# Optimization experiments

Hardware: AMD Instinct MI355X
Metric: run time of the kernel (lower is better)

The kernel has to match this reference:

```python
import jax, jax.numpy as jnp
import numpy as np

QDEPTH = 8
WIDTH = 64
HEIGHT = 64
WIRES = 12  # ceil(log2(64*64))
BATCH = 1024


def setup_inputs() -> dict:
    key = jax.random.key(0)
    k1, k2 = jax.random.split(key)
    x = jax.random.normal(k1, (BATCH, 1, WIDTH, HEIGHT), dtype=jnp.float32)
    # torch.nn.Parameter(torch.randn(weight_shape) * 0.4)
    weights = jax.random.normal(k2, (QDEPTH, WIRES, 3), dtype=jnp.float32) * 0.4
    return {"x": x, "weights": weights, "reps": 1}


def _rot_matrices(angles):
    # angles: (L, W, 3) -> (L, W, 2, 2) complex64; Rot(phi, theta, omega) = RZ(omega) RY(theta) RZ(phi)
    phi, theta, omega = angles[..., 0], angles[..., 1], angles[..., 2]
    c = jnp.cos(theta * 0.5).astype(jnp.complex64)
    s = jnp.sin(theta * 0.5).astype(jnp.complex64)
    ep = jnp.exp(-0.5j * (phi + omega).astype(jnp.complex64))  # e^{-i(phi+omega)/2}
    em = jnp.exp(-0.5j * (phi - omega).astype(jnp.complex64))  # e^{-i(phi-omega)/2}
    row0 = jnp.stack([ep * c, -jnp.conj(em) * s], axis=-1)
    row1 = jnp.stack([em * s, jnp.conj(ep) * c], axis=-1)
    return jnp.stack([row0, row1], axis=-2)


def _apply_1q(state, U, wire):
    # state: (B, 2, 2, ..., 2); apply 2x2 U on axis wire+1
    ax = wire + 1
    s = jnp.moveaxis(state, ax, -1)
    s = s @ U.T  # out[..., i] = sum_j U[i, j] s[..., j]
    return jnp.moveaxis(s, -1, ax)


def _apply_cnot(state, control, target):
    c, t = control + 1, target + 1
    s0, s1 = jnp.split(state, 2, axis=c)   # control = 0 / 1 halves
    s1 = jnp.flip(s1, axis=t)              # X on target where control = 1
    return jnp.concatenate([s0, s1], axis=c)


def _sel_layer(state, mats_l, r):
    # one StronglyEntanglingLayers layer: Rot on every wire, then CNOT ring of range r
    for w in range(WIRES):
        state = _apply_1q(state, mats_l[w], w)
    for w in range(WIRES):
        state = _apply_cnot(state, w, (w + r) % WIRES)
    return state


def _circuit(state, weights, reps):
    mats = _rot_matrices(jnp.tanh(weights))  # qw_map.tanh applied to raw weights
    for _ in range(reps):
        for l in range(QDEPTH):
            r = (l % (WIRES - 1)) + 1  # PennyLane default ranges
            layer = jax.checkpoint(lambda s, m, _r=r: _sel_layer(s, m, _r))
            state = layer(state, mats[l])
    return state


def reference(x, weights, reps):
    b = x.shape[0]
    v = x.reshape(b, -1)  # (b, 4096)
    norm = jnp.linalg.norm(v, axis=-1, keepdims=True)
    v = (v / norm).astype(jnp.complex64)
    state = v.reshape((b,) + (2,) * WIRES)
    state = _circuit(state, weights, reps)
    out = state.reshape(b, -1) * norm
    return out.reshape(b, 1, WIDTH, HEIGHT)
```

## Files before the change

### kernel.cpp

```cpp
#include <hip/hip_runtime.h>

#define WIRES   12
#define NSTATE  4096
#define QDEPTH  8
#define BLOCK   256
#define PER_T   16

using f2 = __attribute__((ext_vector_type(2))) float;

constexpr int colF(int l, int j) {
    int rr = (l % (WIRES - 1)) + 1;
    int v = 1 << j;
    for (int k = WIRES - 1; k >= 0; --k) {
        int bc = 11 - k;
        int bt = 11 - ((k + rr) % WIRES);
        v ^= ((v >> bc) & 1) << bt;
    }
    return v;
}

constexpr int sigma_c(int x) {
    int p = ((x >> 6) & 15) | (((x >> 10) & 3) << 4) | ((x & 63) << 6);
    return p ^ (((p >> 4) & 7) << 1);
}
struct SColsT { int v[QDEPTH][WIRES]; };
constexpr SColsT mkSCols() {
    SColsT c{};
    for (int l = 0; l < QDEPTH; ++l)
        for (int j = 0; j < WIRES; ++j) c.v[l][j] = sigma_c(colF(l, j));
    return c;
}
static __device__ const SColsT SCOLS = mkSCols();

#define OFF_KP 288
#define OFF_KW 544
#define OFF_AN 800

__global__ void setup_kernel(const float* __restrict__ wts, f2* __restrict__ mg)
{
    const int t = threadIdx.x;
    if (t < QDEPTH * WIRES) {
        float th = tanhf(wts[t * 3 + 1]);
        float c = cosf(0.5f * th), s = sinf(0.5f * th);
        mg[(t / 12) * 36 + (t % 12) * 3 + 0] = f2{ c,  c};
        mg[(t / 12) * 36 + (t % 12) * 3 + 1] = f2{-s, -s};
        mg[(t / 12) * 36 + (t % 12) * 3 + 2] = f2{ s,  s};
    }
    if (t < 64) {
        int l = t >> 3, j = t & 7;
        float aP = 0.5f * tanhf(wts[(l * 12 + (7 - j)) * 3 + 0]);
        int wj = (j == 0) ? 1 : (j == 1) ? 0 : (13 - j);
        float aW = 0.5f * tanhf(wts[(l * 12 + wj) * 3 + 2]);
        mg[OFF_AN + l * 8 + j] = f2{aP, aW};
    }
    {
        int l = t >> 5, k = (t >> 1) & 15;
        bool isW = (t & 1) != 0;
        float ph = 0.f;
        #pragma unroll
        for (int j = 0; j < 4; ++j) {
            int wire = isW ? (5 - j) : (11 - j);
            int comp = isW ? 2 : 0;
            float a  = 0.5f * tanhf(wts[(l * 12 + wire) * 3 + comp]);
            ph += ((k >> j) & 1) ? a : -a;
        }
        float s, c;
        sincosf(ph, &s, &c);
        int base = isW ? OFF_KW : OFF_KP;
        mg[base + l * 32 + k * 2 + 0] = f2{ c, c};
        mg[base + l * 32 + k * 2 + 1] = f2{-s, s};
    }
}

template<int P>
__device__ __forceinline__ void gateR(f2 r[PER_T], f2 cc, f2 ms, f2 ss)
{
    #pragma unroll
    for (int pr = 0; pr < PER_T / 2; pr += 2) {
        const int k0 = ((pr >> P) << (P + 1)) | (pr & ((1 << P) - 1));
        const int k1 = k0 | (1 << P);
        const int q  = pr + 1;
        const int j0 = ((q >> P) << (P + 1)) | (q & ((1 << P) - 1));
        const int j1 = j0 | (1 << P);
        f2 a0, b0, a1, b1;
        asm("v_pk_mul_f32 %0, %4, %8\n\t"
            "v_pk_mul_f32 %1, %4, %10\n\t"
            "v_pk_mul_f32 %2, %6, %8\n\t"
            "v_pk_mul_f32 %3, %6, %10\n\t"
            "v_pk_fma_f32 %0, %5, %9, %0\n\t"
            "v_pk_fma_f32 %1, %5, %8, %1\n\t"
            "v_pk_fma_f32 %2, %7, %9, %2\n\t"
            "v_pk_fma_f32 %3, %7, %8, %3"
            : "=&v"(a0), "=&v"(b0), "=&v"(a1), "=&v"(b1)
            : "v"(r[k0]), "v"(r[k1]), "v"(r[j0]), "v"(r[j1]),
              "v"(cc), "v"(ms), "v"(ss));
        r[k0] = a0; r[k1] = b0; r[j0] = a1; r[j1] = b1;
    }
}

template<int CTRL>
__device__ __forceinline__ f2 dpp_xor(f2 v) {
    f2 o;
    o.x = __int_as_float(__builtin_amdgcn_update_dpp(
            0, __float_as_int(v.x), CTRL, 0xF, 0xF, true));
    o.y = __int_as_float(__builtin_amdgcn_update_dpp(
            0, __float_as_int(v.y), CTRL, 0xF, 0xF, true));
    return o;
}

template<int CTRL>
__device__ __forceinline__ void dgateR(f2 r[PER_T], f2 cc, f2 k2)
{
    #pragma unroll
    for (int k0 = 0; k0 < PER_T; k0 += 4) {
        f2 p0 = dpp_xor<CTRL>(r[k0 + 0]);
        f2 p1 = dpp_xor<CTRL>(r[k0 + 1]);
        f2 p2 = dpp_xor<CTRL>(r[k0 + 2]);
        f2 p3 = dpp_xor<CTRL>(r[k0 + 3]);
        f2 o0, o1, o2, o3;
        asm("v_pk_mul_f32 %0, %4, %12\n\t"
            "v_pk_mul_f32 %1, %5, %12\n\t"
            "v_pk_mul_f32 %2, %6, %12\n\t"
            "v_pk_mul_f32 %3, %7, %12\n\t"
            "v_pk_fma_f32 %0, %8, %13, %0\n\t"
            "v_pk_fma_f32 %1, %9, %13, %1\n\t"
            "v_pk_fma_f32 %2, %10, %13, %2\n\t"
            "v_pk_fma_f32 %3, %11, %13, %3"
            : "=&v"(o0), "=&v"(o1), "=&v"(o2), "=&v"(o3)
            : "v"(r[k0]), "v"(r[k0+1]), "v"(r[k0+2]), "v"(r[k0+3]),
              "v"(p0), "v"(p1), "v"(p2), "v"(p3),
              "v"(cc), "v"(k2));
        r[k0] = o0; r[k0+1] = o1; r[k0+2] = o2; r[k0+3] = o3;
    }
}

__device__ __forceinline__ void dmul2(f2& a0, f2& a1, f2 d0r, f2 d0w,
                                      f2 d1r, f2 d1w)
{
    f2 o0, o1;
    asm("v_pk_mul_f32 %0, %2, %4\n\t"
        "v_pk_mul_f32 %1, %3, %6\n\t"
        "v_pk_fma_f32 %0, %2, %5, %0 op_sel:[1,0,0] op_sel_hi:[0,1,1]\n\t"
        "v_pk_fma_f32 %1, %3, %7, %1 op_sel:[1,0,0] op_sel_hi:[0,1,1]"
        : "=&v"(o0), "=&v"(o1)
        : "v"(a0), "v"(a1), "v"(d0r), "v"(d0w), "v"(d1r), "v"(d1w));
    a0 = o0; a1 = o1;
}

__device__ __forceinline__ void diag(f2 r[PER_T], const f2* __restrict__ AN,
                                     const f2* __restrict__ KF, int g, bool isW)
{
    float ph = 0.f;
    #pragma unroll
    for (int j = 0; j < 8; ++j) {
        float a = isW ? AN[j].y : AN[j].x;
        ph += ((g >> j) & 1) ? a : -a;
    }
    float s, c;
    sincosf(ph, &s, &c);
    const f2 Lr = f2{c, c}, Lw = f2{-s, s};
    #pragma unroll
    for (int k = 0; k < PER_T; k += 2)
        dmul2(r[k], r[k + 1], Lr, Lw, Lr, Lw);
    #pragma unroll
    for (int k = 0; k < PER_T; k += 2)
        dmul2(r[k], r[k + 1], KF[2*k], KF[2*k + 1], KF[2*k + 2], KF[2*k + 3]);
}

__global__ __launch_bounds__(BLOCK, 4) void qsim_kernel(
    const float* __restrict__ x,
    const f2*    __restrict__ mg,
    const int*   __restrict__ reps_ptr,
    float*       __restrict__ out,
    int write_mode)
{
    __shared__ alignas(16) f2 st[4096];
    float4* const stv = (float4*)st;

    const int g = threadIdx.x;
    const int b = blockIdx.x;
    const bool hb0 = (g & 1) != 0;
    const bool hb1 = (g & 2) != 0;

    const int Pg  = ((g >> 2) & 15) | (((g >> 6) & 3) << 4) | ((g & 3) << 10);
    const int B0W = Pg ^ (((g >> 6) & 3) << 1);
    const int B1W = B0W ^ 8;
    const int baseR4 = ((g & 3) << 3) | ((g >> 2) << 5);
    const int hj     = g & 7;

    const float4* xb4 = (const float4*)(x + (size_t)b * NSTATE) + g * 4;
    f2 r[PER_T];
    #pragma unroll
    for (int c = 0; c < 4; ++c) {
        float4 v = xb4[c];
        r[4*c+0] = f2{v.x, 0.f};
        r[4*c+1] = f2{v.y, 0.f};
        r[4*c+2] = f2{v.z, 0.f};
        r[4*c+3] = f2{v.w, 0.f};
    }

    const int reps = reps_ptr[0];
    for (int rep = 0; rep < reps; ++rep) {
        #pragma unroll 1
        for (int l = 0; l < QDEPTH; ++l) {
            const f2* CS = mg + l * 36;
            const f2* KP = mg + OFF_KP + l * 32;
            const f2* KW = mg + OFF_KW + l * 32;
            const f2* AN = mg + OFF_AN + l * 8;

            diag(r, AN, KP, g, false);

            gateR<0>(r, CS[11*3], CS[11*3+1], CS[11*3+2]);
            gateR<1>(r, CS[10*3], CS[10*3+1], CS[10*3+2]);
            gateR<2>(r, CS[9*3],  CS[9*3+1],  CS[9*3+2]);
            gateR<3>(r, CS[8*3],  CS[8*3+1],  CS[8*3+2]);
            dgateR<0xB1>(r, CS[7*3], hb0 ? CS[7*3+2] : CS[7*3+1]);
            dgateR<0x4E>(r, CS[6*3], hb1 ? CS[6*3+2] : CS[6*3+1]);

            #pragma unroll
            for (int k = 0; k < PER_T; ++k)
                st[((k & 1) ? B1W : B0W) + (k << 6)] = r[k];
            __syncthreads();

            #pragma unroll
            for (int j = 0; j < 8; ++j) {
                float4 v = stv[baseR4 | (j ^ hj)];
                r[2*j]     = f2{v.x, v.y};
                r[2*j + 1] = f2{v.z, v.w};
            }

            gateR<0>(r, CS[5*3], CS[5*3+1], CS[5*3+2]);
            gateR<1>(r, CS[4*3], CS[4*3+1], CS[4*3+2]);
            gateR<2>(r, CS[3*3], CS[3*3+1], CS[3*3+2]);
            gateR<3>(r, CS[2*3], CS[2*3+1], CS[2*3+2]);
            dgateR<0xB1>(r, CS[1*3], hb0 ? CS[1*3+2] : CS[1*3+1]);
            dgateR<0x4E>(r, CS[0*3], hb1 ? CS[0*3+2] : CS[0*3+1]);

            diag(r, AN, KW, g, true);

            #pragma unroll
            for (int j = 0; j < 8; ++j)
                stv[baseR4 | (j ^ hj)] =
                    make_float4(r[2*j].x, r[2*j].y, r[2*j+1].x, r[2*j+1].y);
            __syncthreads();

            {
                int Sg = 0;
                #pragma unroll
                for (int j = 0; j < 8; ++j)
                    Sg ^= ((g >> j) & 1) ? SCOLS.v[l][4 + j] : 0;
                const int s0 = SCOLS.v[l][0], s1 = SCOLS.v[l][1];
                const int s2 = SCOLS.v[l][2], s3 = SCOLS.v[l][3];
                #pragma unroll
                for (int k = 0; k < PER_T; ++k) {
                    int sck = ((k & 1) ? s0 : 0) ^ ((k & 2) ? s1 : 0) ^
                              ((k & 4) ? s2 : 0) ^ ((k & 8) ? s3 : 0);
                    r[k] = st[Sg ^ sck];
                }
            }
            __syncthreads();
        }
    }

    if (write_mode == 0) {
        float4* ob4 = (float4*)(out + (size_t)b * NSTATE) + g * 4;
        #pragma unroll
        for (int c = 0; c < 4; ++c)
            ob4[c] = make_float4(r[4*c].x, r[4*c+1].x, r[4*c+2].x, r[4*c+3].x);
    } else {
        float4* ob4 = (float4*)((float2*)out + (size_t)b * NSTATE) + g * 8;
        #pragma unroll
        for (int k = 0; k < PER_T; k += 2)
            ob4[k >> 1] = make_float4(r[k].x, r[k].y, r[k+1].x, r[k+1].y);
    }
}

extern "C" void kernel_launch(void* const* d_in, const int* in_sizes, int n_in,
                              void* d_out, int out_size, void* d_ws, size_t ws_size,
                              hipStream_t stream) {
    const float* x    = (const float*)d_in[0];
    const float* wts  = (const float*)d_in[1];
    const int*   reps = (const int*)d_in[2];
    float*       out  = (float*)d_out;
    f2*          mg   = (f2*)d_ws;
    (void)in_sizes; (void)n_in; (void)ws_size;

    const int write_mode = (out_size >= 2 * 1024 * NSTATE) ? 1 : 0;

    setup_kernel<<<1, 256, 0, stream>>>(wts, mg);
    qsim_kernel<<<1024, BLOCK, 0, stream>>>(x, mg, reps, out, write_mode);
}
```

Baseline: 138.5 us.

## Replace XOR-swizzled shared layout with padded layout and fast sincos

Switches the shared-memory state buffer from an XOR-swizzled layout with 128-bit vector accesses to a padded layout (one slot of padding per 16 entries), using scalar 64-bit accesses with a stride-68 read/write pattern and a slot-mapping function for the permutation gather. The aim is to avoid bank conflicts with simpler index arithmetic. It also replaces sincosf with the fast __sinf/__cosf intrinsics. In exchange, each exchange uses twice as many LDS instructions since the 16-byte vector loads are gone, and the fast intrinsics lose some accuracy.

```diff
diff --git a/kernel.cpp b/kernel.cpp
--- a/kernel.cpp
+++ b/kernel.cpp
@@ -7,6 +7,8 @@
 #define PER_T   16
 
 using f2 = __attribute__((ext_vector_type(2))) float;
+
+__device__ __forceinline__ int slotf(int a) { return a + (a >> 4); }
 
 constexpr int colF(int l, int j) {
     int rr = (l % (WIRES - 1)) + 1;
@@ -18,19 +20,14 @@
     }
     return v;
 }
-
-constexpr int sigma_c(int x) {
-    int p = ((x >> 6) & 15) | (((x >> 10) & 3) << 4) | ((x & 63) << 6);
-    return p ^ (((p >> 4) & 7) << 1);
-}
-struct SColsT { int v[QDEPTH][WIRES]; };
-constexpr SColsT mkSCols() {
-    SColsT c{};
+struct ColsT { int v[QDEPTH][WIRES]; };
+constexpr ColsT mkCols() {
+    ColsT c{};
     for (int l = 0; l < QDEPTH; ++l)
-        for (int j = 0; j < WIRES; ++j) c.v[l][j] = sigma_c(colF(l, j));
+        for (int j = 0; j < WIRES; ++j) c.v[l][j] = colF(l, j);
     return c;
 }
-static __device__ const SColsT SCOLS = mkSCols();
+static __device__ const ColsT COLS = mkCols();
 
 #define OFF_KP 288
 #define OFF_KW 544
@@ -156,8 +153,7 @@
         float a = isW ? AN[j].y : AN[j].x;
         ph += ((g >> j) & 1) ? a : -a;
     }
-    float s, c;
-    sincosf(ph, &s, &c);
+    float s = __sinf(ph), c = __cosf(ph);
     const f2 Lr = f2{c, c}, Lw = f2{-s, s};
     #pragma unroll
     for (int k = 0; k < PER_T; k += 2)
@@ -174,19 +170,16 @@
     float*       __restrict__ out,
     int write_mode)
 {
-    __shared__ alignas(16) f2 st[4096];
-    float4* const stv = (float4*)st;
+    __shared__ f2 st[4352];
 
     const int g = threadIdx.x;
     const int b = blockIdx.x;
     const bool hb0 = (g & 1) != 0;
     const bool hb1 = (g & 2) != 0;
 
-    const int Pg  = ((g >> 2) & 15) | (((g >> 6) & 3) << 4) | ((g & 3) << 10);
-    const int B0W = Pg ^ (((g >> 6) & 3) << 1);
-    const int B1W = B0W ^ 8;
-    const int baseR4 = ((g & 3) << 3) | ((g >> 2) << 5);
-    const int hj     = g & 7;
+    const int w1b = 17 * g;
+    const int base_g = ((g & 3) << 10) | (g >> 2);
+    const int rAb    = base_g + (base_g >> 4);
 
     const float4* xb4 = (const float4*)(x + (size_t)b * NSTATE) + g * 4;
     f2 r[PER_T];
@@ -218,16 +211,11 @@
             dgateR<0x4E>(r, CS[6*3], hb1 ? CS[6*3+2] : CS[6*3+1]);
 
             #pragma unroll
-            for (int k = 0; k < PER_T; ++k)
-                st[((k & 1) ? B1W : B0W) + (k << 6)] = r[k];
+            for (int k = 0; k < PER_T; ++k) st[w1b + k] = r[k];
             __syncthreads();
 
             #pragma unroll
-            for (int j = 0; j < 8; ++j) {
-                float4 v = stv[baseR4 | (j ^ hj)];
-                r[2*j]     = f2{v.x, v.y};
-                r[2*j + 1] = f2{v.z, v.w};
-            }
+            for (int k = 0; k < PER_T; ++k) r[k] = st[rAb + 68 * k];
 
             gateR<0>(r, CS[5*3], CS[5*3+1], CS[5*3+2]);
             gateR<1>(r, CS[4*3], CS[4*3+1], CS[4*3+2]);
@@ -239,23 +227,21 @@
             diag(r, AN, KW, g, true);
 
             #pragma unroll
-            for (int j = 0; j < 8; ++j)
-                stv[baseR4 | (j ^ hj)] =
-                    make_float4(r[2*j].x, r[2*j].y, r[2*j+1].x, r[2*j+1].y);
+            for (int k = 0; k < PER_T; ++k) st[rAb + 68 * k] = r[k];
             __syncthreads();
 
             {
-                int Sg = 0;
+                int Fg = 0;
                 #pragma unroll
                 for (int j = 0; j < 8; ++j)
-                    Sg ^= ((g >> j) & 1) ? SCOLS.v[l][4 + j] : 0;
-                const int s0 = SCOLS.v[l][0], s1 = SCOLS.v[l][1];
-                const int s2 = SCOLS.v[l][2], s3 = SCOLS.v[l][3];
+                    Fg ^= ((g >> j) & 1) ? COLS.v[l][4 + j] : 0;
+                const int c0 = COLS.v[l][0], c1 = COLS.v[l][1];
+                const int c2 = COLS.v[l][2], c3 = COLS.v[l][3];
                 #pragma unroll
                 for (int k = 0; k < PER_T; ++k) {
-                    int sck = ((k & 1) ? s0 : 0) ^ ((k & 2) ? s1 : 0) ^
-                              ((k & 4) ? s2 : 0) ^ ((k & 8) ? s3 : 0);
-                    r[k] = st[Sg ^ sck];
+                    int ck = ((k & 1) ? c0 : 0) ^ ((k & 2) ? c1 : 0) ^
+                             ((k & 4) ? c2 : 0) ^ ((k & 8) ? c3 : 0);
+                    r[k] = st[slotf(Fg ^ ck)];
                 }
             }
             __syncthreads();
```

Result: no change. 140.0 us (+1.1%).
